# Kernel optimization log

Hardware: AMD Instinct MI355X
Metric: run time of the kernel (lower is better)

## Reference

```python
import jax, jax.numpy as jnp
import numpy as np

B, C, H, W, TF, NH = 16, 512, 24, 24, 512, 8
CPH = C // NH  # channels per head = 64


def setup_inputs() -> dict:
    key = jax.random.key(0)
    ks = jax.random.split(key, 10)
    s = 0.02
    return {
        "x": jax.random.normal(ks[0], (B, C, H, W), jnp.float32),
        "t": jax.random.normal(ks[1], (B, TF), jnp.float32),
        "Wk": jax.random.normal(ks[2], (C, C), jnp.float32) * s,      # 1x1 conv, no bias
        "Wq": jax.random.normal(ks[3], (C, C), jnp.float32) * s,      # 1x1 conv, no bias
        "Wt_w": jax.random.normal(ks[4], (C, TF), jnp.float32) * s,   # Linear weight (out,in)
        "Wt_b": jnp.zeros((C,), jnp.float32),
        "Wm": jax.random.normal(ks[5], (C, C + TF), jnp.float32) * s, # merge 1x1 conv, no bias
        "Wv": jax.random.normal(ks[6], (C, C), jnp.float32) * s,      # 1x1 conv, no bias
        "Wr_w": jax.random.normal(ks[7], (C, C), jnp.float32) * s,    # 1x1 conv with bias
        "Wr_b": jnp.zeros((C,), jnp.float32),
    }


def reference(x, t, Wk, Wq, Wt_w, Wt_b, Wm, Wv, Wr_w, Wr_b):
    b, c, h, w = x.shape
    hw = h * w
    scale = 1.0 / np.sqrt(CPH).astype(np.float32)

    # broadcast text features spatially and merge with image features (1x1 conv)
    t_r = jnp.broadcast_to(t[:, :, None, None], (b, t.shape[1], h, w))
    vl = jnp.einsum('oc,bchw->bohw', Wm, jnp.concatenate([x, t_r], axis=1))
    values = jnp.einsum('oc,bchw->bohw', Wv, vl).reshape(b, NH, CPH, hw)

    # self-attention map: softmax over keys (last dim)
    keys = jnp.einsum('oc,bchw->bohw', Wk, x).reshape(b, NH, CPH, hw)
    queries = jnp.einsum('oc,bchw->bohw', Wq, x).reshape(b, NH, CPH, hw)
    self_att = jax.nn.softmax(
        jnp.einsum('bhcn,bhcm->bhnm', queries, keys) * scale, axis=-1)

    # global cross-attention map: text query vs spatial positions, softmax over hw
    t_m = (t @ Wt_w.T + Wt_b).reshape(b, NH, CPH)
    cross = jax.nn.softmax(
        jnp.einsum('bhcm,bhc->bhm', x.reshape(b, NH, CPH, hw), t_m) * scale, axis=-1)

    # additive combination, then value-weighted aggregation
    att = self_att + cross[:, :, None, :]                    # [b, nh, hw_q, hw_k]
    out = jnp.einsum('bhcm,bhnm->bhcn', values, att).reshape(b, c, h, w)
    out = jnp.einsum('oc,bchw->bohw', Wr_w, out) + Wr_b[None, :, None, None]
    return out
```

## Files before the change

### kernel.cpp

```cpp
#include <hip/hip_runtime.h>
#include <cstdint>
#include <cstddef>

#define NB    16
#define NC    512
#define NHW   576
#define NTF   512
#define NHEAD 8
#define NCPH  64
#define NTOT  9216
#define ATT_SCALE 0.125f
#define SCALE_L2E 0.18033688011112042f

typedef float  floatx4 __attribute__((ext_vector_type(4)));
typedef short  short8  __attribute__((ext_vector_type(8)));
typedef unsigned short ushortx4 __attribute__((ext_vector_type(4)));

__device__ __forceinline__ unsigned short f2bf(float f) {
    unsigned int u = __float_as_uint(f);
    u += 0x7fffu + ((u >> 16) & 1u);
    return (unsigned short)(u >> 16);
}
__device__ __forceinline__ float bf2f(unsigned short h) {
    return __uint_as_float(((unsigned int)h) << 16);
}


__global__ void k_prep_weights(const float* __restrict__ Wq, const float* __restrict__ Wk,
                               const float* __restrict__ Wm, const float* __restrict__ Wv,
                               const float* __restrict__ Wr,
                               unsigned short* __restrict__ Wqkm,
                               unsigned short* __restrict__ Wv_bf,
                               unsigned short* __restrict__ Wr_bf) {
    int i = blockIdx.x * 256 + threadIdx.x;
    if (i < 1536 * 512) {
        int r = i >> 9, c = i & 511;
        float v;
        if (r < 512)       v = Wq[r * 512 + c];
        else if (r < 1024) v = Wk[(r - 512) * 512 + c];
        else               v = Wm[(size_t)(r - 1024) * 1024 + c];
        Wqkm[i] = f2bf(v);
    } else {
        int j = i - 1536 * 512;
        if (j < 512 * 512) Wv_bf[j] = f2bf(Wv[j]);
        else               Wr_bf[j - 512 * 512] = f2bf(Wr[j - 512 * 512]);
    }
}

__global__ void k_prep_xT(const float* __restrict__ x, unsigned short* __restrict__ xT) {
    __shared__ float tile[32][33];
    int b  = blockIdx.z;
    int p0 = blockIdx.x * 32, c0 = blockIdx.y * 32;
    int tx = threadIdx.x, ty = threadIdx.y;
    const float* xb = x + (size_t)b * NC * NHW;
    #pragma unroll
    for (int k = 0; k < 4; k++)
        tile[ty + k * 8][tx] = xb[(size_t)(c0 + ty + k * 8) * NHW + p0 + tx];
    __syncthreads();
    unsigned short* xTb = xT + (size_t)b * NHW * NC;
    #pragma unroll
    for (int k = 0; k < 4; k++)
        xTb[(size_t)(p0 + ty + k * 8) * NC + c0 + tx] = f2bf(tile[tx][ty + k * 8]);
}

__global__ void k_prep_t(const float* __restrict__ t, const float* __restrict__ Wt_w,
                         const float* __restrict__ Wt_b, const float* __restrict__ Wm,
                         float* __restrict__ tm, float* __restrict__ tmerge) {
    __shared__ float ts[512];
    int b = blockIdx.x;
    int tid = threadIdx.x;
    ts[tid]       = t[b * 512 + tid];
    ts[tid + 256] = t[b * 512 + tid + 256];
    __syncthreads();
    int oo = blockIdx.y * 256 + tid;
    const float* Wrow = (oo < 512) ? (Wt_w + (size_t)oo * 512)
                                   : (Wm + (size_t)(oo - 512) * 1024 + 512);
    float acc = 0.f;
    #pragma unroll 4
    for (int c = 0; c < 512; c += 4) {
        float4 w = *reinterpret_cast<const float4*>(Wrow + c);
        acc += w.x * ts[c] + w.y * ts[c + 1] + w.z * ts[c + 2] + w.w * ts[c + 3];
    }
    if (oo < 512) tm[b * 512 + oo] = acc + Wt_b[oo];
    else          tmerge[b * 512 + (oo - 512)] = acc;
}


__device__ __forceinline__ void g128_stage(const unsigned short* __restrict__ src,
                                           unsigned short* lds, int tid) {
    int row  = tid >> 3;
    int slot = (tid & 7) ^ (row & 7);
    #pragma unroll
    for (int i = 0; i < 4; i++) {
        __builtin_amdgcn_global_load_lds(
            (const __attribute__((address_space(1))) unsigned int*)(src + (size_t)(32 * i + row) * NC + slot * 8),
            (__attribute__((address_space(3))) unsigned int*)(lds + i * 2048 + tid * 8), 16, 0, 0);
    }
}

__device__ __forceinline__ void g128_main(const unsigned short* __restrict__ Asrc,
                                          const unsigned short* __restrict__ Bsrc,
                                          unsigned short (*At)[8192], unsigned short (*Bt)[8192],
                                          int tid, int lane, int wr, int wc,
                                          floatx4 (&acc)[4][4]) {
    int cl = lane & 15, hi = lane >> 4, sx = cl & 7;

    g128_stage(Asrc, At[0], tid);
    g128_stage(Bsrc, Bt[0], tid);
    __syncthreads();

    int buf = 0;
    for (int ks = 0; ks < 8; ks++) {
        if (ks < 7) {
            g128_stage(Asrc + (ks + 1) * 64, At[buf ^ 1], tid);
            g128_stage(Bsrc + (ks + 1) * 64, Bt[buf ^ 1], tid);
        }
        #pragma unroll
        for (int kk = 0; kk < 2; kk++) {
            int sl = ((kk << 2) + hi) ^ sx;
            short8 a[4], bb[4];
            #pragma unroll
            for (int i = 0; i < 4; i++)
                a[i] = *reinterpret_cast<const short8*>(&At[buf][(wr * 64 + i * 16 + cl) * 64 + sl * 8]);
            #pragma unroll
            for (int j = 0; j < 4; j++)
                bb[j] = *reinterpret_cast<const short8*>(&Bt[buf][(wc * 64 + j * 16 + cl) * 64 + sl * 8]);
            #pragma unroll
            for (int i = 0; i < 4; i++)
                #pragma unroll
                for (int j = 0; j < 4; j++)
                    acc[i][j] = __builtin_amdgcn_mfma_f32_16x16x32_bf16(a[i], bb[j], acc[i][j], 0, 0, 0);
        }
        __syncthreads();
        buf ^= 1;
    }
}

__global__ void k_gemm_qkm(const unsigned short* __restrict__ Wqkm,
                           const unsigned short* __restrict__ xT,
                           const float* __restrict__ tmerge,
                           unsigned short* __restrict__ QT,
                           unsigned short* __restrict__ KT,
                           unsigned short* __restrict__ vlT) {
    __shared__ unsigned short At[2][8192], Bt[2][8192];
    int tid = threadIdx.x, lane = tid & 63, wid = tid >> 6;
    int wr = wid >> 1, wc = wid & 1;
    int bid = blockIdx.x;
    int xcd = bid & 7, slot = bid >> 3;
    int m = slot / 9, nl = slot % 9;
    int n0 = (xcd * 9 + nl) * 128;
    int o0 = m * 128;

    floatx4 acc[4][4];
    floatx4 zz = {0.f, 0.f, 0.f, 0.f};
    #pragma unroll
    for (int i = 0; i < 4; i++)
        #pragma unroll
        for (int j = 0; j < 4; j++) acc[i][j] = zz;

    g128_main(Wqkm + (size_t)o0 * NC, xT + (size_t)n0 * NC, At, Bt, tid, lane, wr, wc, acc);

    unsigned short* Yt;
    bool addm = false;
    if (m < 4)      Yt = QT;
    else if (m < 8) Yt = KT;
    else          { Yt = vlT; addm = true; }
    int ob = (m & 3) * 128 + wr * 64;

    int cl = lane & 15, r0 = (lane >> 4) * 4;
    #pragma unroll
    for (int i = 0; i < 4; i++) {
        int ol = ob + i * 16 + r0;
        #pragma unroll
        for (int jn = 0; jn < 4; jn++) {
            int n = n0 + wc * 64 + jn * 16 + cl;
            float a0 = 0.f, a1 = 0.f, a2 = 0.f, a3 = 0.f;
            if (addm) {
                int b = n / NHW;
                float4 tv = *reinterpret_cast<const float4*>(tmerge + b * NC + ol);
                a0 = tv.x; a1 = tv.y; a2 = tv.z; a3 = tv.w;
            }
            ushortx4 pk;
            pk[0] = f2bf(acc[i][jn][0] + a0);
            pk[1] = f2bf(acc[i][jn][1] + a1);
            pk[2] = f2bf(acc[i][jn][2] + a2);
            pk[3] = f2bf(acc[i][jn][3] + a3);
            *reinterpret_cast<ushortx4*>(Yt + (size_t)n * NC + ol) = pk;
        }
    }
}

__global__ void k_gemm_v(const unsigned short* __restrict__ Wv_bf,
                         const unsigned short* __restrict__ vlT,
                         unsigned short* __restrict__ V) {
    __shared__ unsigned short At[2][8192], Bt[2][8192];
    int tid = threadIdx.x, lane = tid & 63, wid = tid >> 6;
    int wr = wid >> 1, wc = wid & 1;
    int bid = blockIdx.x;
    int xcd = bid & 7, slot = bid >> 3;
    int m = slot / 9, nl = slot % 9;
    int n0 = (xcd * 9 + nl) * 128;
    int o0 = m * 128;

    floatx4 acc[4][4];
    floatx4 zz = {0.f, 0.f, 0.f, 0.f};
    #pragma unroll
    for (int i = 0; i < 4; i++)
        #pragma unroll
        for (int j = 0; j < 4; j++) acc[i][j] = zz;

    g128_main(Wv_bf + (size_t)o0 * NC, vlT + (size_t)n0 * NC, At, Bt, tid, lane, wr, wc, acc);

    int cl = lane & 15, r0 = (lane >> 4) * 4;
    #pragma unroll
    for (int i = 0; i < 4; i++)
        #pragma unroll
        for (int jn = 0; jn < 4; jn++) {
            int n = n0 + wc * 64 + jn * 16 + cl;
            int b = n / NHW, p = n - b * NHW;
            #pragma unroll
            for (int j = 0; j < 4; j++) {
                int c = o0 + wr * 64 + i * 16 + r0 + j;
                V[((size_t)b * NC + c) * NHW + p] = f2bf(acc[i][jn][j]);
            }
        }
}

__global__ void k_gemm_final(const unsigned short* __restrict__ Wr_bf,
                             const unsigned short* __restrict__ AO,
                             const float* __restrict__ Wr_b,
                             float* __restrict__ out) {
    __shared__ unsigned short At[2][8192], Bt[2][8192];
    int tid = threadIdx.x, lane = tid & 63, wid = tid >> 6;
    int wr = wid >> 1, wc = wid & 1;
    int bid = blockIdx.x;
    int xcd = bid & 7, slot = bid >> 3;
    int m = slot / 9, nl = slot % 9;
    int n0 = (xcd * 9 + nl) * 128;
    int o0 = m * 128;

    floatx4 acc[4][4];
    floatx4 zz = {0.f, 0.f, 0.f, 0.f};
    #pragma unroll
    for (int i = 0; i < 4; i++)
        #pragma unroll
        for (int j = 0; j < 4; j++) acc[i][j] = zz;

    g128_main(Wr_bf + (size_t)o0 * NC, AO + (size_t)n0 * NC, At, Bt, tid, lane, wr, wc, acc);

    int cl = lane & 15, r0 = (lane >> 4) * 4;
    #pragma unroll
    for (int i = 0; i < 4; i++) {
        float4 bv = *reinterpret_cast<const float4*>(Wr_b + o0 + wr * 64 + i * 16 + r0);
        float bias[4] = {bv.x, bv.y, bv.z, bv.w};
        #pragma unroll
        for (int jn = 0; jn < 4; jn++) {
            int n = n0 + wc * 64 + jn * 16 + cl;
            int b = n / NHW, p = n - b * NHW;
            #pragma unroll
            for (int j = 0; j < 4; j++) {
                int c = o0 + wr * 64 + i * 16 + r0 + j;
                out[((size_t)b * NC + c) * NHW + p] = acc[i][jn][j] + bias[j];
            }
        }
    }
}


__global__ void k_cross_o2(const unsigned short* __restrict__ xT,
                           const unsigned short* __restrict__ V,
                           const float* __restrict__ tm,
                           float* __restrict__ o2) {
    __shared__ float tms[64];
    __shared__ float ss[576];
    __shared__ float red[8];
    __shared__ float part[4][64];
    int bh = blockIdx.x;
    int b = bh >> 3, h = bh & 7;
    int tid = threadIdx.x;

    if (tid < 64) tms[tid] = tm[b * 512 + h * 64 + tid];
    __syncthreads();

    for (int m = tid; m < 576; m += 256) {
        const short8* xr8 = reinterpret_cast<const short8*>(xT + ((size_t)b * NHW + m) * NC + h * 64);
        float acc = 0.f;
        #pragma unroll
        for (int cc = 0; cc < 8; cc++) {
            short8 v8 = xr8[cc];
            #pragma unroll
            for (int q = 0; q < 8; q++)
                acc += bf2f((unsigned short)v8[q]) * tms[cc * 8 + q];
        }
        ss[m] = acc * ATT_SCALE;
    }
    __syncthreads();

    float pmax = -3e38f;
    for (int m = tid; m < 576; m += 256) pmax = fmaxf(pmax, ss[m]);
    #pragma unroll
    for (int off = 32; off; off >>= 1) pmax = fmaxf(pmax, __shfl_xor(pmax, off));
    if ((tid & 63) == 0) red[tid >> 6] = pmax;
    __syncthreads();
    float mx = fmaxf(fmaxf(red[0], red[1]), fmaxf(red[2], red[3]));

    float psum = 0.f;
    for (int m = tid; m < 576; m += 256) {
        float e = __expf(ss[m] - mx);
        ss[m] = e;
        psum += e;
    }
    #pragma unroll
    for (int off = 32; off; off >>= 1) psum += __shfl_xor(psum, off);
    if ((tid & 63) == 0) red[4 + (tid >> 6)] = psum;
    __syncthreads();
    float inv = 1.f / (red[4] + red[5] + red[6] + red[7]);

    int c = tid & 63, seg = tid >> 6;
    const unsigned short* vr = V + ((size_t)b * NC + h * 64 + c) * NHW;
    float pa = 0.f;
    for (int m = seg * 144; m < seg * 144 + 144; m++) pa += bf2f(vr[m]) * ss[m];
    part[seg][c] = pa;
    __syncthreads();
    if (tid < 64)
        o2[(b * 8 + h) * 64 + tid] =
            (part[0][tid] + part[1][tid] + part[2][tid] + part[3][tid]) * inv;
}


__global__ void k_attn(const unsigned short* __restrict__ QT,
                       const unsigned short* __restrict__ KT,
                       const unsigned short* __restrict__ V,
                       const float* __restrict__ o2,
                       unsigned short* __restrict__ AO) {
    __shared__ unsigned short Ktile[2][64][64];
    __shared__ unsigned short Vtile[2][64][64];
    __shared__ unsigned short pbuf[4][16][88];
    int tid  = threadIdx.x;
    int lane = tid & 63, wid = tid >> 6;

    int bid  = blockIdx.x;
    int xcd  = bid & 7;
    int slot = bid >> 3;
    int bh   = xcd * 16 + slot / 9;
    int qt   = slot % 9;
    int b = bh >> 3, h = bh & 7;
    int n0 = qt * 64 + wid * 16;
    int cl = lane & 15;
    int r0 = (lane >> 4) * 4;
    int part = lane >> 4;
    int ko = part * 8;

    const unsigned short* Qb = QT + ((size_t)b * NHW + n0) * NC + h * 64;
    const unsigned short* Kb = KT + (size_t)b * NHW * NC + h * 64;
    const unsigned short* Vb = V  + ((size_t)b * NC + h * 64) * NHW;

    short8 aq0 = *reinterpret_cast<const short8*>(Qb + (size_t)cl * NC + ko);
    short8 aq1 = *reinterpret_cast<const short8*>(Qb + (size_t)cl * NC + 32 + ko);

    int srow = lane >> 3;
    int scol = (lane & 7) ^ srow;

    floatx4 zz = {0.f, 0.f, 0.f, 0.f};
    floatx4 oacc[4] = {zz, zz, zz, zz};
    float es[4] = {0.f, 0.f, 0.f, 0.f};

    {
        const unsigned short* ks = Kb + (size_t)(wid * 16 + srow) * NC + scol * 8;
        const unsigned short* vs = Vb + (size_t)(wid * 16 + srow) * NHW + scol * 8;
        #pragma unroll
        for (int i = 0; i < 2; i++) {
            __builtin_amdgcn_global_load_lds(
                (const __attribute__((address_space(1))) unsigned int*)(ks + (size_t)i * 8 * NC),
                (__attribute__((address_space(3))) unsigned int*)&Ktile[0][wid * 16 + i * 8][0], 16, 0, 0);
            __builtin_amdgcn_global_load_lds(
                (const __attribute__((address_space(1))) unsigned int*)(vs + (size_t)i * 8 * NHW),
                (__attribute__((address_space(3))) unsigned int*)&Vtile[0][wid * 16 + i * 8][0], 16, 0, 0);
        }
    }
    __syncthreads();

    int buf = 0;
    for (int chk = 0; chk < 9; chk++) {
        int m0 = chk * 64;
        if (chk < 8) {
            const unsigned short* ks = Kb + (size_t)(m0 + 64 + wid * 16 + srow) * NC + scol * 8;
            const unsigned short* vs = Vb + (size_t)(wid * 16 + srow) * NHW + (m0 + 64) + scol * 8;
            #pragma unroll
            for (int i = 0; i < 2; i++) {
                __builtin_amdgcn_global_load_lds(
                    (const __attribute__((address_space(1))) unsigned int*)(ks + (size_t)i * 8 * NC),
                    (__attribute__((address_space(3))) unsigned int*)&Ktile[buf ^ 1][wid * 16 + i * 8][0], 16, 0, 0);
                __builtin_amdgcn_global_load_lds(
                    (const __attribute__((address_space(1))) unsigned int*)(vs + (size_t)i * 8 * NHW),
                    (__attribute__((address_space(3))) unsigned int*)&Vtile[buf ^ 1][wid * 16 + i * 8][0], 16, 0, 0);
            }
        }

        floatx4 s[4];
        #pragma unroll
        for (int t = 0; t < 4; t++) {
            int row = t * 16 + cl;
            int sw = cl & 7;
            short8 bk0 = *reinterpret_cast<const short8*>(&Ktile[buf][row][(part ^ sw) * 8]);
            short8 bk1 = *reinterpret_cast<const short8*>(&Ktile[buf][row][((part + 4) ^ sw) * 8]);
            s[t] = __builtin_amdgcn_mfma_f32_16x16x32_bf16(aq0, bk0, zz, 0, 0, 0);
            s[t] = __builtin_amdgcn_mfma_f32_16x16x32_bf16(aq1, bk1, s[t], 0, 0, 0);
        }
        #pragma unroll
        for (int t = 0; t < 4; t++)
            #pragma unroll
            for (int j = 0; j < 4; j++) {
                float e = exp2f(s[t][j] * SCALE_L2E);
                es[j] += e;
                pbuf[wid][r0 + j][t * 16 + cl] = f2bf(e);
            }
        short8 pa0 = *reinterpret_cast<const short8*>(&pbuf[wid][cl][ko]);
        short8 pa1 = *reinterpret_cast<const short8*>(&pbuf[wid][cl][32 + ko]);
        #pragma unroll
        for (int ct = 0; ct < 4; ct++) {
            int row = ct * 16 + cl;
            int sw = cl & 7;
            short8 bv0 = *reinterpret_cast<const short8*>(&Vtile[buf][row][(part ^ sw) * 8]);
            short8 bv1 = *reinterpret_cast<const short8*>(&Vtile[buf][row][((part + 4) ^ sw) * 8]);
            oacc[ct] = __builtin_amdgcn_mfma_f32_16x16x32_bf16(pa0, bv0, oacc[ct], 0, 0, 0);
            oacc[ct] = __builtin_amdgcn_mfma_f32_16x16x32_bf16(pa1, bv1, oacc[ct], 0, 0, 0);
        }
        __syncthreads();
        buf ^= 1;
    }

    #pragma unroll
    for (int off = 1; off < 16; off <<= 1)
        #pragma unroll
        for (int j = 0; j < 4; j++) es[j] += __shfl_xor(es[j], off);
    float ri[4];
    #pragma unroll
    for (int j = 0; j < 4; j++) ri[j] = 1.f / es[j];

    const float* o2b = o2 + bh * 64;
    #pragma unroll
    for (int ct = 0; ct < 4; ct++) {
        float o2v = o2b[ct * 16 + cl];
        #pragma unroll
        for (int j = 0; j < 4; j++)
            pbuf[wid][r0 + j][ct * 16 + cl] = f2bf(oacc[ct][j] * ri[j] + o2v);
    }
    short8 w0 = *reinterpret_cast<const short8*>(&pbuf[wid][cl][part * 16]);
    short8 w1 = *reinterpret_cast<const short8*>(&pbuf[wid][cl][part * 16 + 8]);
    unsigned short* dst = AO + ((size_t)b * NHW + n0 + cl) * NC + h * 64 + part * 16;
    *reinterpret_cast<short8*>(dst)     = w0;
    *reinterpret_cast<short8*>(dst + 8) = w1;
}


extern "C" void kernel_launch(void* const* d_in, const int* in_sizes, int n_in,
                              void* d_out, int out_size, void* d_ws, size_t ws_size,
                              hipStream_t stream) {
    const float* x    = (const float*)d_in[0];
    const float* t    = (const float*)d_in[1];
    const float* Wk   = (const float*)d_in[2];
    const float* Wq   = (const float*)d_in[3];
    const float* Wt_w = (const float*)d_in[4];
    const float* Wt_b = (const float*)d_in[5];
    const float* Wm   = (const float*)d_in[6];
    const float* Wv   = (const float*)d_in[7];
    const float* Wr_w = (const float*)d_in[8];
    const float* Wr_b = (const float*)d_in[9];
    float* out = (float*)d_out;
    char* ws = (char*)d_ws;

    unsigned short* xT    = (unsigned short*)(ws);
    unsigned short* Wqkm  = (unsigned short*)(ws + 9437184);
    unsigned short* Wv_bf = (unsigned short*)(ws + 11010048);
    unsigned short* Wr_bf = (unsigned short*)(ws + 11534336);
    float*          tm     = (float*)(ws + 12058624);
    float*          tmerge = (float*)(ws + 12091392);
    unsigned short* QT    = (unsigned short*)(ws + 12124160);
    unsigned short* KT    = (unsigned short*)(ws + 21561344);
    unsigned short* vlT   = (unsigned short*)(ws + 30998528);
    unsigned short* Vv    = (unsigned short*)(ws + 40435712);
    float*          o2    = (float*)(ws + 49872896);
    unsigned short* AO    = xT;
    (void)in_sizes; (void)n_in; (void)out_size; (void)ws_size;

    k_prep_weights<<<5120, 256, 0, stream>>>(Wq, Wk, Wm, Wv, Wr_w, Wqkm, Wv_bf, Wr_bf);
    k_prep_xT<<<dim3(18, 16, 16), dim3(32, 8), 0, stream>>>(x, xT);
    k_prep_t<<<dim3(16, 4), 256, 0, stream>>>(t, Wt_w, Wt_b, Wm, tm, tmerge);
    k_gemm_qkm<<<864, 256, 0, stream>>>(Wqkm, xT, tmerge, QT, KT, vlT);
    k_gemm_v<<<288, 256, 0, stream>>>(Wv_bf, vlT, Vv);
    k_cross_o2<<<128, 256, 0, stream>>>(xT, Vv, tm, o2);
    k_attn<<<1152, 256, 0, stream>>>(QT, KT, Vv, o2, AO);
    k_gemm_final<<<288, 256, 0, stream>>>(Wr_bf, AO, Wr_b, out);
}
```

Baseline: 124.7 us.

## Fold Wv into merge weights and widen attention tiles to 32 queries per wave

Precomputes Wv·Wm as a fused weight matrix, with a small GEMM kernel applied to weights only, so the values come straight out of the QKM GEMM. This removes the separate value GEMM and the vlT intermediate round trip. The attention kernel now runs 6 waves per block with two 16-row query tiles per wave, so each staged K/V tile is reused across more queries and there are fewer blocks. The fold adds a weight-side GEMM every call and an extra bf16 rounding of the product weights, and the doubled accumulators raise register pressure in the attention kernel.

Result: slower. 137.8 us (+10.5%).

```diff
diff --git a/kernel.cpp b/kernel.cpp
--- a/kernel.cpp
+++ b/kernel.cpp
@@ -8,7 +8,6 @@
 #define NTF   512
 #define NHEAD 8
 #define NCPH  64
-#define NTOT  9216
 #define ATT_SCALE 0.125f
 #define SCALE_L2E 0.18033688011112042f
 
@@ -27,24 +26,33 @@
 
 
 __global__ void k_prep_weights(const float* __restrict__ Wq, const float* __restrict__ Wk,
-                               const float* __restrict__ Wm, const float* __restrict__ Wv,
-                               const float* __restrict__ Wr,
+                               const float* __restrict__ Wv, const float* __restrict__ Wr,
                                unsigned short* __restrict__ Wqkm,
                                unsigned short* __restrict__ Wv_bf,
                                unsigned short* __restrict__ Wr_bf) {
     int i = blockIdx.x * 256 + threadIdx.x;
-    if (i < 1536 * 512) {
+    if (i < 1024 * 512) {
         int r = i >> 9, c = i & 511;
-        float v;
-        if (r < 512)       v = Wq[r * 512 + c];
-        else if (r < 1024) v = Wk[(r - 512) * 512 + c];
-        else               v = Wm[(size_t)(r - 1024) * 1024 + c];
+        float v = (r < 512) ? Wq[r * 512 + c] : Wk[(r - 512) * 512 + c];
         Wqkm[i] = f2bf(v);
     } else {
-        int j = i - 1536 * 512;
+        int j = i - 1024 * 512;
         if (j < 512 * 512) Wv_bf[j] = f2bf(Wv[j]);
         else               Wr_bf[j - 512 * 512] = f2bf(Wr[j - 512 * 512]);
     }
+}
+
+__global__ void k_prep_wmT(const float* __restrict__ Wm, unsigned short* __restrict__ WmT) {
+    __shared__ float tile[32][33];
+    int n0 = blockIdx.x * 32, k0 = blockIdx.y * 32;
+    int tx = threadIdx.x, ty = threadIdx.y;
+    #pragma unroll
+    for (int k = 0; k < 4; k++)
+        tile[ty + k * 8][tx] = Wm[(size_t)(k0 + ty + k * 8) * 1024 + n0 + tx];
+    __syncthreads();
+    #pragma unroll
+    for (int k = 0; k < 4; k++)
+        WmT[(size_t)(n0 + ty + k * 8) * 512 + k0 + tx] = f2bf(tile[tx][ty + k * 8]);
 }
 
 __global__ void k_prep_xT(const float* __restrict__ x, unsigned short* __restrict__ xT) {
@@ -64,7 +72,7 @@
 }
 
 __global__ void k_prep_t(const float* __restrict__ t, const float* __restrict__ Wt_w,
-                         const float* __restrict__ Wt_b, const float* __restrict__ Wm,
+                         const float* __restrict__ Wt_b, const float* __restrict__ Wvm_txt,
                          float* __restrict__ tm, float* __restrict__ tmerge) {
     __shared__ float ts[512];
     int b = blockIdx.x;
@@ -74,7 +82,7 @@
     __syncthreads();
     int oo = blockIdx.y * 256 + tid;
     const float* Wrow = (oo < 512) ? (Wt_w + (size_t)oo * 512)
-                                   : (Wm + (size_t)(oo - 512) * 1024 + 512);
+                                   : (Wvm_txt + (size_t)(oo - 512) * 512);
     float acc = 0.f;
     #pragma unroll 4
     for (int c = 0; c < 512; c += 4) {
@@ -136,12 +144,46 @@
     }
 }
 
+__global__ void k_fold(const unsigned short* __restrict__ Wv_bf,
+                       const unsigned short* __restrict__ WmT,
+                       unsigned short* __restrict__ Wqkm,
+                       float* __restrict__ Wvm_txt) {
+    __shared__ unsigned short At[2][8192], Bt[2][8192];
+    int tid = threadIdx.x, lane = tid & 63, wid = tid >> 6;
+    int wr = wid >> 1, wc = wid & 1;
+    int m = blockIdx.x >> 3, nt = blockIdx.x & 7;
+    int o0 = m * 128, n0 = nt * 128;
+
+    floatx4 acc[4][4];
+    floatx4 zz = {0.f, 0.f, 0.f, 0.f};
+    #pragma unroll
+    for (int i = 0; i < 4; i++)
+        #pragma unroll
+        for (int j = 0; j < 4; j++) acc[i][j] = zz;
+
+    g128_main(Wv_bf + (size_t)o0 * NC, WmT + (size_t)n0 * NC, At, Bt, tid, lane, wr, wc, acc);
+
+    int cl = lane & 15, r0 = (lane >> 4) * 4;
+    #pragma unroll
+    for (int i = 0; i < 4; i++)
+        #pragma unroll
+        for (int jn = 0; jn < 4; jn++) {
+            int n = n0 + wc * 64 + jn * 16 + cl;
+            #pragma unroll
+            for (int j = 0; j < 4; j++) {
+                int o = o0 + wr * 64 + i * 16 + r0 + j;
+                if (n0 < 512) Wqkm[(size_t)(1024 + o) * 512 + n] = f2bf(acc[i][jn][j]);
+                else          Wvm_txt[(size_t)o * 512 + (n - 512)] = acc[i][jn][j];
+            }
+        }
+}
+
 __global__ void k_gemm_qkm(const unsigned short* __restrict__ Wqkm,
                            const unsigned short* __restrict__ xT,
                            const float* __restrict__ tmerge,
                            unsigned short* __restrict__ QT,
                            unsigned short* __restrict__ KT,
-                           unsigned short* __restrict__ vlT) {
+                           unsigned short* __restrict__ V) {
     __shared__ unsigned short At[2][8192], Bt[2][8192];
     int tid = threadIdx.x, lane = tid & 63, wid = tid >> 6;
     int wr = wid >> 1, wc = wid & 1;
@@ -160,70 +202,41 @@
 
     g128_main(Wqkm + (size_t)o0 * NC, xT + (size_t)n0 * NC, At, Bt, tid, lane, wr, wc, acc);
 
-    unsigned short* Yt;
-    bool addm = false;
-    if (m < 4)      Yt = QT;
-    else if (m < 8) Yt = KT;
-    else          { Yt = vlT; addm = true; }
+    int cl = lane & 15, r0 = (lane >> 4) * 4;
     int ob = (m & 3) * 128 + wr * 64;
 
-    int cl = lane & 15, r0 = (lane >> 4) * 4;
-    #pragma unroll
-    for (int i = 0; i < 4; i++) {
-        int ol = ob + i * 16 + r0;
-        #pragma unroll
-        for (int jn = 0; jn < 4; jn++) {
-            int n = n0 + wc * 64 + jn * 16 + cl;
-            float a0 = 0.f, a1 = 0.f, a2 = 0.f, a3 = 0.f;
-            if (addm) {
-                int b = n / NHW;
+    if (m < 8) {
+        unsigned short* Yt = (m < 4) ? QT : KT;
+        #pragma unroll
+        for (int i = 0; i < 4; i++) {
+            int ol = ob + i * 16 + r0;
+            #pragma unroll
+            for (int jn = 0; jn < 4; jn++) {
+                int n = n0 + wc * 64 + jn * 16 + cl;
+                ushortx4 pk;
+                pk[0] = f2bf(acc[i][jn][0]);
+                pk[1] = f2bf(acc[i][jn][1]);
+                pk[2] = f2bf(acc[i][jn][2]);
+                pk[3] = f2bf(acc[i][jn][3]);
+                *reinterpret_cast<ushortx4*>(Yt + (size_t)n * NC + ol) = pk;
+            }
+        }
+    } else {
+        #pragma unroll
+        for (int i = 0; i < 4; i++) {
+            int ol = ob + i * 16 + r0;
+            #pragma unroll
+            for (int jn = 0; jn < 4; jn++) {
+                int n = n0 + wc * 64 + jn * 16 + cl;
+                int b = n / NHW, p = n - b * NHW;
                 float4 tv = *reinterpret_cast<const float4*>(tmerge + b * NC + ol);
-                a0 = tv.x; a1 = tv.y; a2 = tv.z; a3 = tv.w;
+                float bias[4] = {tv.x, tv.y, tv.z, tv.w};
+                #pragma unroll
+                for (int j = 0; j < 4; j++)
+                    V[((size_t)b * NC + ol + j) * NHW + p] = f2bf(acc[i][jn][j] + bias[j]);
             }
-            ushortx4 pk;
-            pk[0] = f2bf(acc[i][jn][0] + a0);
-            pk[1] = f2bf(acc[i][jn][1] + a1);
-            pk[2] = f2bf(acc[i][jn][2] + a2);
-            pk[3] = f2bf(acc[i][jn][3] + a3);
-            *reinterpret_cast<ushortx4*>(Yt + (size_t)n * NC + ol) = pk;
-        }
-    }
-}
-
-__global__ void k_gemm_v(const unsigned short* __restrict__ Wv_bf,
-                         const unsigned short* __restrict__ vlT,
-                         unsigned short* __restrict__ V) {
-    __shared__ unsigned short At[2][8192], Bt[2][8192];
-    int tid = threadIdx.x, lane = tid & 63, wid = tid >> 6;
-    int wr = wid >> 1, wc = wid & 1;
-    int bid = blockIdx.x;
-    int xcd = bid & 7, slot = bid >> 3;
-    int m = slot / 9, nl = slot % 9;
-    int n0 = (xcd * 9 + nl) * 128;
-    int o0 = m * 128;
-
-    floatx4 acc[4][4];
-    floatx4 zz = {0.f, 0.f, 0.f, 0.f};
-    #pragma unroll
-    for (int i = 0; i < 4; i++)
-        #pragma unroll
-        for (int j = 0; j < 4; j++) acc[i][j] = zz;
-
-    g128_main(Wv_bf + (size_t)o0 * NC, vlT + (size_t)n0 * NC, At, Bt, tid, lane, wr, wc, acc);
-
-    int cl = lane & 15, r0 = (lane >> 4) * 4;
-    #pragma unroll
-    for (int i = 0; i < 4; i++)
-        #pragma unroll
-        for (int jn = 0; jn < 4; jn++) {
-            int n = n0 + wc * 64 + jn * 16 + cl;
-            int b = n / NHW, p = n - b * NHW;
-            #pragma unroll
-            for (int j = 0; j < 4; j++) {
-                int c = o0 + wr * 64 + i * 16 + r0 + j;
-                V[((size_t)b * NC + c) * NHW + p] = f2bf(acc[i][jn][j]);
-            }
-        }
+        }
+    }
 }
 
 __global__ void k_gemm_final(const unsigned short* __restrict__ Wr_bf,
@@ -328,103 +341,111 @@
 }
 
 
-__global__ void k_attn(const unsigned short* __restrict__ QT,
+__global__ __launch_bounds__(384) void k_attn(
+                       const unsigned short* __restrict__ QT,
                        const unsigned short* __restrict__ KT,
                        const unsigned short* __restrict__ V,
                        const float* __restrict__ o2,
                        unsigned short* __restrict__ AO) {
     __shared__ unsigned short Ktile[2][64][64];
     __shared__ unsigned short Vtile[2][64][64];
-    __shared__ unsigned short pbuf[4][16][88];
+    __shared__ unsigned short pbuf[6][32][72];
     int tid  = threadIdx.x;
     int lane = tid & 63, wid = tid >> 6;
 
     int bid  = blockIdx.x;
     int xcd  = bid & 7;
     int slot = bid >> 3;
-    int bh   = xcd * 16 + slot / 9;
-    int qt   = slot % 9;
+    int bh   = xcd * 16 + slot / 3;
+    int qt   = slot % 3;
     int b = bh >> 3, h = bh & 7;
-    int n0 = qt * 64 + wid * 16;
+    int base = qt * 192 + wid * 32;
     int cl = lane & 15;
-    int r0 = (lane >> 4) * 4;
-    int part = lane >> 4;
-    int ko = part * 8;
-
-    const unsigned short* Qb = QT + ((size_t)b * NHW + n0) * NC + h * 64;
+    int hi = lane >> 4;
+    int r0 = hi * 4;
+    int ko = hi * 8;
+    int sw = cl & 7;
+
+    const unsigned short* Qb = QT + ((size_t)b * NHW + base) * NC + h * 64;
     const unsigned short* Kb = KT + (size_t)b * NHW * NC + h * 64;
     const unsigned short* Vb = V  + ((size_t)b * NC + h * 64) * NHW;
 
-    short8 aq0 = *reinterpret_cast<const short8*>(Qb + (size_t)cl * NC + ko);
-    short8 aq1 = *reinterpret_cast<const short8*>(Qb + (size_t)cl * NC + 32 + ko);
-
-    int srow = lane >> 3;
-    int scol = (lane & 7) ^ srow;
+    short8 aq0a = *reinterpret_cast<const short8*>(Qb + (size_t)cl * NC + ko);
+    short8 aq1a = *reinterpret_cast<const short8*>(Qb + (size_t)cl * NC + 32 + ko);
+    short8 aq0b = *reinterpret_cast<const short8*>(Qb + (size_t)(16 + cl) * NC + ko);
+    short8 aq1b = *reinterpret_cast<const short8*>(Qb + (size_t)(16 + cl) * NC + 32 + ko);
+
+    int row1 = tid >> 3;
+    int sl1  = (tid & 7) ^ (row1 & 7);
+    int row2 = 48 + (tid >> 3);
+    int sl2  = (tid & 7) ^ (row2 & 7);
 
     floatx4 zz = {0.f, 0.f, 0.f, 0.f};
-    floatx4 oacc[4] = {zz, zz, zz, zz};
-    float es[4] = {0.f, 0.f, 0.f, 0.f};
-
-    {
-        const unsigned short* ks = Kb + (size_t)(wid * 16 + srow) * NC + scol * 8;
-        const unsigned short* vs = Vb + (size_t)(wid * 16 + srow) * NHW + scol * 8;
-        #pragma unroll
-        for (int i = 0; i < 2; i++) {
-            __builtin_amdgcn_global_load_lds(
-                (const __attribute__((address_space(1))) unsigned int*)(ks + (size_t)i * 8 * NC),
-                (__attribute__((address_space(3))) unsigned int*)&Ktile[0][wid * 16 + i * 8][0], 16, 0, 0);
-            __builtin_amdgcn_global_load_lds(
-                (const __attribute__((address_space(1))) unsigned int*)(vs + (size_t)i * 8 * NHW),
-                (__attribute__((address_space(3))) unsigned int*)&Vtile[0][wid * 16 + i * 8][0], 16, 0, 0);
-        }
-    }
+    floatx4 oaccA[4] = {zz, zz, zz, zz};
+    floatx4 oaccB[4] = {zz, zz, zz, zz};
+    float esA[4] = {0.f, 0.f, 0.f, 0.f};
+    float esB[4] = {0.f, 0.f, 0.f, 0.f};
+
+#define STAGE_KV(m0, bb)                                                                              \
+    {                                                                                                 \
+        __builtin_amdgcn_global_load_lds(                                                             \
+            (const __attribute__((address_space(1))) unsigned int*)(Kb + (size_t)((m0) + row1) * NC + sl1 * 8), \
+            (__attribute__((address_space(3))) unsigned int*)(&Ktile[bb][0][0] + tid * 8), 16, 0, 0); \
+        __builtin_amdgcn_global_load_lds(                                                             \
+            (const __attribute__((address_space(1))) unsigned int*)(Vb + (size_t)row1 * NHW + (m0) + sl1 * 8), \
+            (__attribute__((address_space(3))) unsigned int*)(&Vtile[bb][0][0] + tid * 8), 16, 0, 0); \
+        if (tid < 128) {                                                                              \
+            __builtin_amdgcn_global_load_lds(                                                         \
+                (const __attribute__((address_space(1))) unsigned int*)(Kb + (size_t)((m0) + row2) * NC + sl2 * 8), \
+                (__attribute__((address_space(3))) unsigned int*)(&Ktile[bb][48][0] + tid * 8), 16, 0, 0); \
+            __builtin_amdgcn_global_load_lds(                                                         \
+                (const __attribute__((address_space(1))) unsigned int*)(Vb + (size_t)row2 * NHW + (m0) + sl2 * 8), \
+                (__attribute__((address_space(3))) unsigned int*)(&Vtile[bb][48][0] + tid * 8), 16, 0, 0); \
+        }                                                                                             \
+    }
+
+    STAGE_KV(0, 0);
     __syncthreads();
 
     int buf = 0;
     for (int chk = 0; chk < 9; chk++) {
-        int m0 = chk * 64;
-        if (chk < 8) {
-            const unsigned short* ks = Kb + (size_t)(m0 + 64 + wid * 16 + srow) * NC + scol * 8;
-            const unsigned short* vs = Vb + (size_t)(wid * 16 + srow) * NHW + (m0 + 64) + scol * 8;
-            #pragma unroll
-            for (int i = 0; i < 2; i++) {
-                __builtin_amdgcn_global_load_lds(
-                    (const __attribute__((address_space(1))) unsigned int*)(ks + (size_t)i * 8 * NC),
-                    (__attribute__((address_space(3))) unsigned int*)&Ktile[buf ^ 1][wid * 16 + i * 8][0], 16, 0, 0);
-                __builtin_amdgcn_global_load_lds(
-                    (const __attribute__((address_space(1))) unsigned int*)(vs + (size_t)i * 8 * NHW),
-                    (__attribute__((address_space(3))) unsigned int*)&Vtile[buf ^ 1][wid * 16 + i * 8][0], 16, 0, 0);
-            }
-        }
-
-        floatx4 s[4];
+        if (chk < 8) STAGE_KV(chk * 64 + 64, buf ^ 1);
+
+        floatx4 sA[4], sB[4];
         #pragma unroll
         for (int t = 0; t < 4; t++) {
             int row = t * 16 + cl;
-            int sw = cl & 7;
-            short8 bk0 = *reinterpret_cast<const short8*>(&Ktile[buf][row][(part ^ sw) * 8]);
-            short8 bk1 = *reinterpret_cast<const short8*>(&Ktile[buf][row][((part + 4) ^ sw) * 8]);
-            s[t] = __builtin_amdgcn_mfma_f32_16x16x32_bf16(aq0, bk0, zz, 0, 0, 0);
-            s[t] = __builtin_amdgcn_mfma_f32_16x16x32_bf16(aq1, bk1, s[t], 0, 0, 0);
+            short8 bk0 = *reinterpret_cast<const short8*>(&Ktile[buf][row][(hi ^ sw) * 8]);
+            short8 bk1 = *reinterpret_cast<const short8*>(&Ktile[buf][row][((hi + 4) ^ sw) * 8]);
+            sA[t] = __builtin_amdgcn_mfma_f32_16x16x32_bf16(aq0a, bk0, zz, 0, 0, 0);
+            sA[t] = __builtin_amdgcn_mfma_f32_16x16x32_bf16(aq1a, bk1, sA[t], 0, 0, 0);
+            sB[t] = __builtin_amdgcn_mfma_f32_16x16x32_bf16(aq0b, bk0, zz, 0, 0, 0);
+            sB[t] = __builtin_amdgcn_mfma_f32_16x16x32_bf16(aq1b, bk1, sB[t], 0, 0, 0);
         }
         #pragma unroll
         for (int t = 0; t < 4; t++)
             #pragma unroll
             for (int j = 0; j < 4; j++) {
-                float e = exp2f(s[t][j] * SCALE_L2E);
-                es[j] += e;
-                pbuf[wid][r0 + j][t * 16 + cl] = f2bf(e);
+                float eA = exp2f(sA[t][j] * SCALE_L2E);
+                float eB = exp2f(sB[t][j] * SCALE_L2E);
+                esA[j] += eA;
+                esB[j] += eB;
+                pbuf[wid][r0 + j][t * 16 + cl]      = f2bf(eA);
+                pbuf[wid][16 + r0 + j][t * 16 + cl] = f2bf(eB);
             }
-        short8 pa0 = *reinterpret_cast<const short8*>(&pbuf[wid][cl][ko]);
-        short8 pa1 = *reinterpret_cast<const short8*>(&pbuf[wid][cl][32 + ko]);
+        short8 pA0 = *reinterpret_cast<const short8*>(&pbuf[wid][cl][ko]);
+        short8 pA1 = *reinterpret_cast<const short8*>(&pbuf[wid][cl][32 + ko]);
+        short8 pB0 = *reinterpret_cast<const short8*>(&pbuf[wid][16 + cl][ko]);
+        short8 pB1 = *reinterpret_cast<const short8*>(&pbuf[wid][16 + cl][32 + ko]);
         #pragma unroll
         for (int ct = 0; ct < 4; ct++) {
             int row = ct * 16 + cl;
-            int sw = cl & 7;
-            short8 bv0 = *reinterpret_cast<const short8*>(&Vtile[buf][row][(part ^ sw) * 8]);
-            short8 bv1 = *reinterpret_cast<const short8*>(&Vtile[buf][row][((part + 4) ^ sw) * 8]);
-            oacc[ct] = __builtin_amdgcn_mfma_f32_16x16x32_bf16(pa0, bv0, oacc[ct], 0, 0, 0);
-            oacc[ct] = __builtin_amdgcn_mfma_f32_16x16x32_bf16(pa1, bv1, oacc[ct], 0, 0, 0);
+            short8 bv0 = *reinterpret_cast<const short8*>(&Vtile[buf][row][(hi ^ sw) * 8]);
+            short8 bv1 = *reinterpret_cast<const short8*>(&Vtile[buf][row][((hi + 4) ^ sw) * 8]);
+            oaccA[ct] = __builtin_amdgcn_mfma_f32_16x16x32_bf16(pA0, bv0, oaccA[ct], 0, 0, 0);
+            oaccA[ct] = __builtin_amdgcn_mfma_f32_16x16x32_bf16(pA1, bv1, oaccA[ct], 0, 0, 0);
+            oaccB[ct] = __builtin_amdgcn_mfma_f32_16x16x32_bf16(pB0, bv0, oaccB[ct], 0, 0, 0);
+            oaccB[ct] = __builtin_amdgcn_mfma_f32_16x16x32_bf16(pB1, bv1, oaccB[ct], 0, 0, 0);
         }
         __syncthreads();
         buf ^= 1;
@@ -433,24 +454,34 @@
     #pragma unroll
     for (int off = 1; off < 16; off <<= 1)
         #pragma unroll
-        for (int j = 0; j < 4; j++) es[j] += __shfl_xor(es[j], off);
-    float ri[4];
-    #pragma unroll
-    for (int j = 0; j < 4; j++) ri[j] = 1.f / es[j];
+        for (int j = 0; j < 4; j++) {
+            esA[j] += __shfl_xor(esA[j], off);
+            esB[j] += __shfl_xor(esB[j], off);
+        }
+    float riA[4], riB[4];
+    #pragma unroll
+    for (int j = 0; j < 4; j++) { riA[j] = 1.f / esA[j]; riB[j] = 1.f / esB[j]; }
 
     const float* o2b = o2 + bh * 64;
     #pragma unroll
     for (int ct = 0; ct < 4; ct++) {
         float o2v = o2b[ct * 16 + cl];
         #pragma unroll
-        for (int j = 0; j < 4; j++)
-            pbuf[wid][r0 + j][ct * 16 + cl] = f2bf(oacc[ct][j] * ri[j] + o2v);
-    }
-    short8 w0 = *reinterpret_cast<const short8*>(&pbuf[wid][cl][part * 16]);
-    short8 w1 = *reinterpret_cast<const short8*>(&pbuf[wid][cl][part * 16 + 8]);
-    unsigned short* dst = AO + ((size_t)b * NHW + n0 + cl) * NC + h * 64 + part * 16;
-    *reinterpret_cast<short8*>(dst)     = w0;
-    *reinterpret_cast<short8*>(dst + 8) = w1;
+        for (int j = 0; j < 4; j++) {
+            pbuf[wid][r0 + j][ct * 16 + cl]      = f2bf(oaccA[ct][j] * riA[j] + o2v);
+            pbuf[wid][16 + r0 + j][ct * 16 + cl] = f2bf(oaccB[ct][j] * riB[j] + o2v);
+        }
+    }
+    unsigned short* dstA = AO + ((size_t)b * NHW + base + cl) * NC + h * 64 + hi * 16;
+    unsigned short* dstB = dstA + (size_t)16 * NC;
+    short8 wA0 = *reinterpret_cast<const short8*>(&pbuf[wid][cl][hi * 16]);
+    short8 wA1 = *reinterpret_cast<const short8*>(&pbuf[wid][cl][hi * 16 + 8]);
+    short8 wB0 = *reinterpret_cast<const short8*>(&pbuf[wid][16 + cl][hi * 16]);
+    short8 wB1 = *reinterpret_cast<const short8*>(&pbuf[wid][16 + cl][hi * 16 + 8]);
+    *reinterpret_cast<short8*>(dstA)     = wA0;
+    *reinterpret_cast<short8*>(dstA + 8) = wA1;
+    *reinterpret_cast<short8*>(dstB)     = wB0;
+    *reinterpret_cast<short8*>(dstB + 8) = wB1;
 }
 
 
@@ -470,26 +501,28 @@
     float* out = (float*)d_out;
     char* ws = (char*)d_ws;
 
-    unsigned short* xT    = (unsigned short*)(ws);
-    unsigned short* Wqkm  = (unsigned short*)(ws + 9437184);
-    unsigned short* Wv_bf = (unsigned short*)(ws + 11010048);
-    unsigned short* Wr_bf = (unsigned short*)(ws + 11534336);
-    float*          tm     = (float*)(ws + 12058624);
-    float*          tmerge = (float*)(ws + 12091392);
-    unsigned short* QT    = (unsigned short*)(ws + 12124160);
-    unsigned short* KT    = (unsigned short*)(ws + 21561344);
-    unsigned short* vlT   = (unsigned short*)(ws + 30998528);
-    unsigned short* Vv    = (unsigned short*)(ws + 40435712);
-    float*          o2    = (float*)(ws + 49872896);
-    unsigned short* AO    = xT;
+    unsigned short* xT      = (unsigned short*)(ws);
+    unsigned short* Wqkm    = (unsigned short*)(ws + 9437184);
+    unsigned short* Wv_bf   = (unsigned short*)(ws + 11010048);
+    unsigned short* Wr_bf   = (unsigned short*)(ws + 11534336);
+    float*          tm      = (float*)(ws + 12058624);
+    float*          tmerge  = (float*)(ws + 12091392);
+    unsigned short* QT      = (unsigned short*)(ws + 12124160);
+    unsigned short* KT      = (unsigned short*)(ws + 21561344);
+    unsigned short* WmT     = (unsigned short*)(ws + 30998528);
+    float*          Wvm_txt = (float*)(ws + 32047104);
+    unsigned short* Vv      = (unsigned short*)(ws + 40435712);
+    float*          o2      = (float*)(ws + 49872896);
+    unsigned short* AO      = xT;
     (void)in_sizes; (void)n_in; (void)out_size; (void)ws_size;
 
-    k_prep_weights<<<5120, 256, 0, stream>>>(Wq, Wk, Wm, Wv, Wr_w, Wqkm, Wv_bf, Wr_bf);
+    k_prep_weights<<<4096, 256, 0, stream>>>(Wq, Wk, Wv, Wr_w, Wqkm, Wv_bf, Wr_bf);
+    k_prep_wmT<<<dim3(32, 16), dim3(32, 8), 0, stream>>>(Wm, WmT);
     k_prep_xT<<<dim3(18, 16, 16), dim3(32, 8), 0, stream>>>(x, xT);
-    k_prep_t<<<dim3(16, 4), 256, 0, stream>>>(t, Wt_w, Wt_b, Wm, tm, tmerge);
-    k_gemm_qkm<<<864, 256, 0, stream>>>(Wqkm, xT, tmerge, QT, KT, vlT);
-    k_gemm_v<<<288, 256, 0, stream>>>(Wv_bf, vlT, Vv);
+    k_fold<<<32, 256, 0, stream>>>(Wv_bf, WmT, Wqkm, Wvm_txt);
+    k_prep_t<<<dim3(16, 4), 256, 0, stream>>>(t, Wt_w, Wt_b, Wvm_txt, tm, tmerge);
+    k_gemm_qkm<<<864, 256, 0, stream>>>(Wqkm, xT, tmerge, QT, KT, Vv);
     k_cross_o2<<<128, 256, 0, stream>>>(xT, Vv, tm, o2);
-    k_attn<<<1152, 256, 0, stream>>>(QT, KT, Vv, o2, AO);
+    k_attn<<<384, 384, 0, stream>>>(QT, KT, Vv, o2, AO);
     k_gemm_final<<<288, 256, 0, stream>>>(Wr_bf, AO, Wr_b, out);
 }
```

## Fold value projection into merge weights to eliminate separate V GEMM

Applied to the files above, without the earlier changes.

Precomputes Wv·Wm on device (image and text halves) with a small GEMM, so the QKM GEMM directly produces V in channel-major layout with a folded text bias. This removes the separate value GEMM over all pixels and the vlT intermediate write/read. It adds a Wm transpose kernel and a fold GEMM each call, and changes rounding since the folded weight is quantized to bf16.

After: 124.4 us. No clear change (-0.3%).

```diff
diff --git a/kernel.cpp b/kernel.cpp
--- a/kernel.cpp
+++ b/kernel.cpp
@@ -8,7 +8,6 @@
 #define NTF   512
 #define NHEAD 8
 #define NCPH  64
-#define NTOT  9216
 #define ATT_SCALE 0.125f
 #define SCALE_L2E 0.18033688011112042f
 
@@ -27,24 +26,33 @@
 
 
 __global__ void k_prep_weights(const float* __restrict__ Wq, const float* __restrict__ Wk,
-                               const float* __restrict__ Wm, const float* __restrict__ Wv,
-                               const float* __restrict__ Wr,
+                               const float* __restrict__ Wv, const float* __restrict__ Wr,
                                unsigned short* __restrict__ Wqkm,
                                unsigned short* __restrict__ Wv_bf,
                                unsigned short* __restrict__ Wr_bf) {
     int i = blockIdx.x * 256 + threadIdx.x;
-    if (i < 1536 * 512) {
+    if (i < 1024 * 512) {
         int r = i >> 9, c = i & 511;
-        float v;
-        if (r < 512)       v = Wq[r * 512 + c];
-        else if (r < 1024) v = Wk[(r - 512) * 512 + c];
-        else               v = Wm[(size_t)(r - 1024) * 1024 + c];
+        float v = (r < 512) ? Wq[r * 512 + c] : Wk[(r - 512) * 512 + c];
         Wqkm[i] = f2bf(v);
     } else {
-        int j = i - 1536 * 512;
+        int j = i - 1024 * 512;
         if (j < 512 * 512) Wv_bf[j] = f2bf(Wv[j]);
         else               Wr_bf[j - 512 * 512] = f2bf(Wr[j - 512 * 512]);
     }
+}
+
+__global__ void k_prep_wmT(const float* __restrict__ Wm, unsigned short* __restrict__ WmT) {
+    __shared__ float tile[32][33];
+    int n0 = blockIdx.x * 32, k0 = blockIdx.y * 32;
+    int tx = threadIdx.x, ty = threadIdx.y;
+    #pragma unroll
+    for (int k = 0; k < 4; k++)
+        tile[ty + k * 8][tx] = Wm[(size_t)(k0 + ty + k * 8) * 1024 + n0 + tx];
+    __syncthreads();
+    #pragma unroll
+    for (int k = 0; k < 4; k++)
+        WmT[(size_t)(n0 + ty + k * 8) * 512 + k0 + tx] = f2bf(tile[tx][ty + k * 8]);
 }
 
 __global__ void k_prep_xT(const float* __restrict__ x, unsigned short* __restrict__ xT) {
@@ -64,7 +72,7 @@
 }
 
 __global__ void k_prep_t(const float* __restrict__ t, const float* __restrict__ Wt_w,
-                         const float* __restrict__ Wt_b, const float* __restrict__ Wm,
+                         const float* __restrict__ Wt_b, const float* __restrict__ Wvm_txt,
                          float* __restrict__ tm, float* __restrict__ tmerge) {
     __shared__ float ts[512];
     int b = blockIdx.x;
@@ -74,7 +82,7 @@
     __syncthreads();
     int oo = blockIdx.y * 256 + tid;
     const float* Wrow = (oo < 512) ? (Wt_w + (size_t)oo * 512)
-                                   : (Wm + (size_t)(oo - 512) * 1024 + 512);
+                                   : (Wvm_txt + (size_t)(oo - 512) * 512);
     float acc = 0.f;
     #pragma unroll 4
     for (int c = 0; c < 512; c += 4) {
@@ -136,12 +144,46 @@
     }
 }
 
+__global__ void k_fold(const unsigned short* __restrict__ Wv_bf,
+                       const unsigned short* __restrict__ WmT,
+                       unsigned short* __restrict__ Wqkm,
+                       float* __restrict__ Wvm_txt) {
+    __shared__ unsigned short At[2][8192], Bt[2][8192];
+    int tid = threadIdx.x, lane = tid & 63, wid = tid >> 6;
+    int wr = wid >> 1, wc = wid & 1;
+    int m = blockIdx.x >> 3, nt = blockIdx.x & 7;
+    int o0 = m * 128, n0 = nt * 128;
+
+    floatx4 acc[4][4];
+    floatx4 zz = {0.f, 0.f, 0.f, 0.f};
+    #pragma unroll
+    for (int i = 0; i < 4; i++)
+        #pragma unroll
+        for (int j = 0; j < 4; j++) acc[i][j] = zz;
+
+    g128_main(Wv_bf + (size_t)o0 * NC, WmT + (size_t)n0 * NC, At, Bt, tid, lane, wr, wc, acc);
+
+    int cl = lane & 15, r0 = (lane >> 4) * 4;
+    #pragma unroll
+    for (int i = 0; i < 4; i++)
+        #pragma unroll
+        for (int jn = 0; jn < 4; jn++) {
+            int n = n0 + wc * 64 + jn * 16 + cl;
+            #pragma unroll
+            for (int j = 0; j < 4; j++) {
+                int o = o0 + wr * 64 + i * 16 + r0 + j;
+                if (n0 < 512) Wqkm[(size_t)(1024 + o) * 512 + n] = f2bf(acc[i][jn][j]);
+                else          Wvm_txt[(size_t)o * 512 + (n - 512)] = acc[i][jn][j];
+            }
+        }
+}
+
 __global__ void k_gemm_qkm(const unsigned short* __restrict__ Wqkm,
                            const unsigned short* __restrict__ xT,
                            const float* __restrict__ tmerge,
                            unsigned short* __restrict__ QT,
                            unsigned short* __restrict__ KT,
-                           unsigned short* __restrict__ vlT) {
+                           unsigned short* __restrict__ V) {
     __shared__ unsigned short At[2][8192], Bt[2][8192];
     int tid = threadIdx.x, lane = tid & 63, wid = tid >> 6;
     int wr = wid >> 1, wc = wid & 1;
@@ -160,70 +202,41 @@
 
     g128_main(Wqkm + (size_t)o0 * NC, xT + (size_t)n0 * NC, At, Bt, tid, lane, wr, wc, acc);
 
-    unsigned short* Yt;
-    bool addm = false;
-    if (m < 4)      Yt = QT;
-    else if (m < 8) Yt = KT;
-    else          { Yt = vlT; addm = true; }
+    int cl = lane & 15, r0 = (lane >> 4) * 4;
     int ob = (m & 3) * 128 + wr * 64;
 
-    int cl = lane & 15, r0 = (lane >> 4) * 4;
-    #pragma unroll
-    for (int i = 0; i < 4; i++) {
-        int ol = ob + i * 16 + r0;
-        #pragma unroll
-        for (int jn = 0; jn < 4; jn++) {
-            int n = n0 + wc * 64 + jn * 16 + cl;
-            float a0 = 0.f, a1 = 0.f, a2 = 0.f, a3 = 0.f;
-            if (addm) {
-                int b = n / NHW;
+    if (m < 8) {
+        unsigned short* Yt = (m < 4) ? QT : KT;
+        #pragma unroll
+        for (int i = 0; i < 4; i++) {
+            int ol = ob + i * 16 + r0;
+            #pragma unroll
+            for (int jn = 0; jn < 4; jn++) {
+                int n = n0 + wc * 64 + jn * 16 + cl;
+                ushortx4 pk;
+                pk[0] = f2bf(acc[i][jn][0]);
+                pk[1] = f2bf(acc[i][jn][1]);
+                pk[2] = f2bf(acc[i][jn][2]);
+                pk[3] = f2bf(acc[i][jn][3]);
+                *reinterpret_cast<ushortx4*>(Yt + (size_t)n * NC + ol) = pk;
+            }
+        }
+    } else {
+        #pragma unroll
+        for (int i = 0; i < 4; i++) {
+            int ol = ob + i * 16 + r0;
+            #pragma unroll
+            for (int jn = 0; jn < 4; jn++) {
+                int n = n0 + wc * 64 + jn * 16 + cl;
+                int b = n / NHW, p = n - b * NHW;
                 float4 tv = *reinterpret_cast<const float4*>(tmerge + b * NC + ol);
-                a0 = tv.x; a1 = tv.y; a2 = tv.z; a3 = tv.w;
+                float bias[4] = {tv.x, tv.y, tv.z, tv.w};
+                #pragma unroll
+                for (int j = 0; j < 4; j++)
+                    V[((size_t)b * NC + ol + j) * NHW + p] = f2bf(acc[i][jn][j] + bias[j]);
             }
-            ushortx4 pk;
-            pk[0] = f2bf(acc[i][jn][0] + a0);
-            pk[1] = f2bf(acc[i][jn][1] + a1);
-            pk[2] = f2bf(acc[i][jn][2] + a2);
-            pk[3] = f2bf(acc[i][jn][3] + a3);
-            *reinterpret_cast<ushortx4*>(Yt + (size_t)n * NC + ol) = pk;
-        }
-    }
-}
-
-__global__ void k_gemm_v(const unsigned short* __restrict__ Wv_bf,
-                         const unsigned short* __restrict__ vlT,
-                         unsigned short* __restrict__ V) {
-    __shared__ unsigned short At[2][8192], Bt[2][8192];
-    int tid = threadIdx.x, lane = tid & 63, wid = tid >> 6;
-    int wr = wid >> 1, wc = wid & 1;
-    int bid = blockIdx.x;
-    int xcd = bid & 7, slot = bid >> 3;
-    int m = slot / 9, nl = slot % 9;
-    int n0 = (xcd * 9 + nl) * 128;
-    int o0 = m * 128;
-
-    floatx4 acc[4][4];
-    floatx4 zz = {0.f, 0.f, 0.f, 0.f};
-    #pragma unroll
-    for (int i = 0; i < 4; i++)
-        #pragma unroll
-        for (int j = 0; j < 4; j++) acc[i][j] = zz;
-
-    g128_main(Wv_bf + (size_t)o0 * NC, vlT + (size_t)n0 * NC, At, Bt, tid, lane, wr, wc, acc);
-
-    int cl = lane & 15, r0 = (lane >> 4) * 4;
-    #pragma unroll
-    for (int i = 0; i < 4; i++)
-        #pragma unroll
-        for (int jn = 0; jn < 4; jn++) {
-            int n = n0 + wc * 64 + jn * 16 + cl;
-            int b = n / NHW, p = n - b * NHW;
-            #pragma unroll
-            for (int j = 0; j < 4; j++) {
-                int c = o0 + wr * 64 + i * 16 + r0 + j;
-                V[((size_t)b * NC + c) * NHW + p] = f2bf(acc[i][jn][j]);
-            }
-        }
+        }
+    }
 }
 
 __global__ void k_gemm_final(const unsigned short* __restrict__ Wr_bf,
@@ -470,25 +483,27 @@
     float* out = (float*)d_out;
     char* ws = (char*)d_ws;
 
-    unsigned short* xT    = (unsigned short*)(ws);
-    unsigned short* Wqkm  = (unsigned short*)(ws + 9437184);
-    unsigned short* Wv_bf = (unsigned short*)(ws + 11010048);
-    unsigned short* Wr_bf = (unsigned short*)(ws + 11534336);
-    float*          tm     = (float*)(ws + 12058624);
-    float*          tmerge = (float*)(ws + 12091392);
-    unsigned short* QT    = (unsigned short*)(ws + 12124160);
-    unsigned short* KT    = (unsigned short*)(ws + 21561344);
-    unsigned short* vlT   = (unsigned short*)(ws + 30998528);
-    unsigned short* Vv    = (unsigned short*)(ws + 40435712);
-    float*          o2    = (float*)(ws + 49872896);
-    unsigned short* AO    = xT;
+    unsigned short* xT      = (unsigned short*)(ws);
+    unsigned short* Wqkm    = (unsigned short*)(ws + 9437184);
+    unsigned short* Wv_bf   = (unsigned short*)(ws + 11010048);
+    unsigned short* Wr_bf   = (unsigned short*)(ws + 11534336);
+    float*          tm      = (float*)(ws + 12058624);
+    float*          tmerge  = (float*)(ws + 12091392);
+    unsigned short* QT      = (unsigned short*)(ws + 12124160);
+    unsigned short* KT      = (unsigned short*)(ws + 21561344);
+    unsigned short* WmT     = (unsigned short*)(ws + 30998528);
+    float*          Wvm_txt = (float*)(ws + 32047104);
+    unsigned short* Vv      = (unsigned short*)(ws + 40435712);
+    float*          o2      = (float*)(ws + 49872896);
+    unsigned short* AO      = xT;
     (void)in_sizes; (void)n_in; (void)out_size; (void)ws_size;
 
-    k_prep_weights<<<5120, 256, 0, stream>>>(Wq, Wk, Wm, Wv, Wr_w, Wqkm, Wv_bf, Wr_bf);
+    k_prep_weights<<<4096, 256, 0, stream>>>(Wq, Wk, Wv, Wr_w, Wqkm, Wv_bf, Wr_bf);
+    k_prep_wmT<<<dim3(32, 16), dim3(32, 8), 0, stream>>>(Wm, WmT);
     k_prep_xT<<<dim3(18, 16, 16), dim3(32, 8), 0, stream>>>(x, xT);
-    k_prep_t<<<dim3(16, 4), 256, 0, stream>>>(t, Wt_w, Wt_b, Wm, tm, tmerge);
-    k_gemm_qkm<<<864, 256, 0, stream>>>(Wqkm, xT, tmerge, QT, KT, vlT);
-    k_gemm_v<<<288, 256, 0, stream>>>(Wv_bf, vlT, Vv);
+    k_fold<<<32, 256, 0, stream>>>(Wv_bf, WmT, Wqkm, Wvm_txt);
+    k_prep_t<<<dim3(16, 4), 256, 0, stream>>>(t, Wt_w, Wt_b, Wvm_txt, tm, tmerge);
+    k_gemm_qkm<<<864, 256, 0, stream>>>(Wqkm, xT, tmerge, QT, KT, Vv);
     k_cross_o2<<<128, 256, 0, stream>>>(xT, Vv, tm, o2);
     k_attn<<<1152, 256, 0, stream>>>(QT, KT, Vv, o2, AO);
     k_gemm_final<<<288, 256, 0, stream>>>(Wr_bf, AO, Wr_b, out);
```
